# Kernel tuning notes

Hardware: AMD Instinct MI355X
Metric: run time of the kernel (lower is better)

The kernel has to match this reference:

```python
import jax, jax.numpy as jnp
import numpy as np

NUM_HEADS = 12
HEAD_SIZE = 64  # hidden 768 / 12 heads


def setup_inputs() -> dict:
    key = jax.random.key(0)
    ks = jax.random.split(key, 5)
    B, M, P, H = 8, 4, 512, 768
    scale = 1.0 / np.sqrt(H)
    return {
        "hidden_states": jax.random.normal(ks[0], (B, M, P, H), dtype=jnp.float32),
        "Wq": jax.random.normal(ks[1], (H, H), dtype=jnp.float32) * scale,
        "bq": jnp.zeros((H,), dtype=jnp.float32),
        "Wk": jax.random.normal(ks[2], (H, H), dtype=jnp.float32) * scale,
        "bk": jnp.zeros((H,), dtype=jnp.float32),
        "Wv": jax.random.normal(ks[3], (H, H), dtype=jnp.float32) * scale,
        "bv": jnp.zeros((H,), dtype=jnp.float32),
        "Wo": jax.random.normal(ks[4], (H, H), dtype=jnp.float32) * scale,
        "bo": jnp.zeros((H,), dtype=jnp.float32),
    }


def reference(hidden_states, Wq, bq, Wk, bk, Wv, bv, Wo, bo):
    # hidden_states: [B, M, P, H] (batch, modalities, patches, hidden)
    B, M, P, H = hidden_states.shape
    nh, hs = NUM_HEADS, HEAD_SIZE

    def split_heads(x):  # [B,M,P,H] -> [B,M,nh,P,hs]
        return x.reshape(B, M, P, nh, hs).transpose(0, 1, 3, 2, 4)

    q = split_heads(hidden_states @ Wq + bq)
    k = split_heads(hidden_states @ Wk + bk)
    v = split_heads(hidden_states @ Wv + bv)

    # per-modality, per-head attention over patches
    scores = jnp.einsum('bmnqh,bmnkh->bmnqk', q, k) / np.sqrt(hs).astype(jnp.float32)
    probs = jax.nn.softmax(scores, axis=-1)  # [B,M,nh,P,P]
    ctx = jnp.einsum('bmnqk,bmnkh->bmnqh', probs, v)
    ctx = ctx.transpose(0, 1, 3, 2, 4).reshape(B, M, P, H)  # merge heads

    # output projection (dropout rate 0.0 -> identity)
    return ctx @ Wo + bo
```

## Files before the change

### kernel.cpp

```cpp
#include <hip/hip_runtime.h>
#include <cstdint>
#include <cstddef>

#define H_DIM 768
#define NHEADS 12
#define HSZ 64
#define PATCH 512
#define MTOT 16384
#define SZT ((long)MTOT * H_DIM)

using short8 = __attribute__((ext_vector_type(8))) short;
using f32x4  = __attribute__((ext_vector_type(4))) float;
using us4    = __attribute__((ext_vector_type(4))) unsigned short;

#define GLL16(gp, lp) __builtin_amdgcn_global_load_lds( \
    (const __attribute__((address_space(1))) void*)(gp), \
    (__attribute__((address_space(3))) void*)(lp), 16, 0, 0)

__device__ __forceinline__ void split_f32(float x, unsigned short& h, unsigned short& l) {
    unsigned u = __float_as_uint(x);
    h = (unsigned short)(u >> 16);
    float rem = __uint_as_float(u & 0xffff0000u);
    float r = x - rem;
    unsigned v = __float_as_uint(r);
    v += 0x7fff + ((v >> 16) & 1);
    l = (unsigned short)(v >> 16);
}

__device__ __forceinline__ unsigned short bf16rne(float x) {
    unsigned v = __float_as_uint(x);
    v += 0x7fff + ((v >> 16) & 1);
    return (unsigned short)(v >> 16);
}

__global__ __launch_bounds__(256) void prep_x(const float* __restrict__ X,
                                              unsigned short* __restrict__ Xb)
{
    const long i = ((long)blockIdx.x * 256 + threadIdx.x) * 8;
    float4 a = *(const float4*)&X[i];
    float4 b = *(const float4*)&X[i + 4];
    float xs[8] = {a.x, a.y, a.z, a.w, b.x, b.y, b.z, b.w};
    us4 h0, h1;
    #pragma unroll
    for (int j = 0; j < 4; ++j) { h0[j] = bf16rne(xs[j]); h1[j] = bf16rne(xs[j + 4]); }
    *(us4*)&Xb[i] = h0; *(us4*)&Xb[i + 4] = h1;
}

template<int LO>
__global__ __launch_bounds__(256) void prep_w(const float* __restrict__ W,
                                              unsigned short* __restrict__ Whi,
                                              unsigned short* __restrict__ Wlo)
{
    __shared__ float T[64][65];
    const int kt = blockIdx.x * 64, nt = blockIdx.y * 64;
    const int tid = threadIdx.x;
    const int r = tid >> 2, c16 = (tid & 3) * 16;
    #pragma unroll
    for (int j = 0; j < 4; ++j) {
        float4 v = *(const float4*)&W[(long)(kt + r) * H_DIM + nt + c16 + j * 4];
        T[r][c16 + j*4 + 0] = v.x; T[r][c16 + j*4 + 1] = v.y;
        T[r][c16 + j*4 + 2] = v.z; T[r][c16 + j*4 + 3] = v.w;
    }
    __syncthreads();
    unsigned short* ph = &Whi[(long)(nt + r) * H_DIM + kt + c16];
    #pragma unroll
    for (int j = 0; j < 16; ++j) {
        if (LO) {
            unsigned short hh, ll;
            split_f32(T[c16 + j][r], hh, ll);
            ph[j] = hh;
            Wlo[(long)(nt + r) * H_DIM + kt + c16 + j] = ll;
        } else {
            ph[j] = bf16rne(T[c16 + j][r]);
        }
    }
}

__global__ __launch_bounds__(256, 2) void qkv_gemm(
    const unsigned short* __restrict__ Xb,
    const unsigned short* __restrict__ WqH, const unsigned short* __restrict__ WkH,
    const unsigned short* __restrict__ WvH,
    const float* __restrict__ bq, const float* __restrict__ bk, const float* __restrict__ bv,
    float qscale,
    unsigned short* __restrict__ Qt, unsigned short* __restrict__ Kp,
    unsigned short* __restrict__ Vp)
{
    __shared__ unsigned short As[16384];
    __shared__ unsigned short Bs[16384];

    const int s   = blockIdx.x + 18 * blockIdx.y;
    const int lid = (s & 7) * 288 + (s >> 3);
    const int bx  = lid % 18;
    const int by  = lid / 18;

    const int mat = bx / 6;
    const int n0  = (bx % 6) * 128;
    const int m0  = by * 128;
    const unsigned short* Bh = (mat == 0) ? WqH : (mat == 1) ? WkH : WvH;
    const float* bias        = (mat == 0) ? bq  : (mat == 1) ? bk  : bv;
    const float scale        = (mat == 0) ? qscale : 1.0f;

    const int tid  = threadIdx.x;
    const int lane = tid & 63;
    const int wv   = tid >> 6;
    const int wr   = wv >> 1, wc = wv & 1;
    const int q    = lane >> 4, l15 = lane & 15;

    const int srow   = tid >> 3;
    const int schunk = (tid & 7) ^ (srow & 7);

    char* ldsA = (char*)(&As[0]) + (wv << 10);
    char* ldsB = (char*)(&Bs[0]) + (wv << 10);

    f32x4 acc[4][4];
    #pragma unroll
    for (int i = 0; i < 4; ++i)
        #pragma unroll
        for (int j = 0; j < 4; ++j) acc[i][j] = 0;

    const int swz = (l15 & 7);

    #pragma unroll
    for (int i = 0; i < 4; ++i) {
        GLL16(Xb + (long)(m0 + i * 32 + srow) * H_DIM + schunk * 8, ldsA + i * 4096);
        GLL16(Bh + (long)(n0 + i * 32 + srow) * H_DIM + schunk * 8, ldsB + i * 4096);
    }

    int kb = 0;
    for (int k0 = 0; k0 < H_DIM; k0 += 64, kb ^= 1) {
        if (k0 + 64 < H_DIM) {
            #pragma unroll
            for (int i = 0; i < 4; ++i) {
                GLL16(Xb + (long)(m0 + i * 32 + srow) * H_DIM + (k0 + 64) + schunk * 8,
                      ldsA + ((kb ^ 1) << 14) + i * 4096);
                GLL16(Bh + (long)(n0 + i * 32 + srow) * H_DIM + (k0 + 64) + schunk * 8,
                      ldsB + ((kb ^ 1) << 14) + i * 4096);
            }
            asm volatile("s_waitcnt vmcnt(8)" ::: "memory");
        } else {
            asm volatile("s_waitcnt vmcnt(0)" ::: "memory");
        }
        __builtin_amdgcn_s_barrier();
        __builtin_amdgcn_sched_barrier(0);

        const unsigned short* Ab = &As[kb << 13];
        const unsigned short* Bb = &Bs[kb << 13];
        #pragma unroll
        for (int ks = 0; ks < 2; ++ks) {
            const int pc = ((ks * 4 + q) ^ swz) * 8;
            short8 ah[4], bh[4];
            #pragma unroll
            for (int t = 0; t < 4; ++t) {
                const int mr = wr * 64 + t * 16 + l15;
                ah[t] = *(const short8*)&Ab[mr * 64 + pc];
                const int nr = wc * 64 + t * 16 + l15;
                bh[t] = *(const short8*)&Bb[nr * 64 + pc];
            }
            #pragma unroll
            for (int mt = 0; mt < 4; ++mt)
                #pragma unroll
                for (int nt = 0; nt < 4; ++nt)
                    acc[mt][nt] = __builtin_amdgcn_mfma_f32_16x16x32_bf16(ah[mt], bh[nt], acc[mt][nt], 0, 0, 0);
        }
        asm volatile("s_waitcnt lgkmcnt(0)" ::: "memory");
        __builtin_amdgcn_sched_barrier(0);
        __builtin_amdgcn_s_barrier();
    }

    #pragma unroll
    for (int nt = 0; nt < 4; ++nt) {
        const int col = n0 + wc * 64 + nt * 16 + l15;
        const float bcol = bias[col];
        const int h = col >> 6, d = col & 63;
        #pragma unroll
        for (int mt = 0; mt < 4; ++mt) {
            const int rowB = m0 + wr * 64 + mt * 16 + q * 4;
            #pragma unroll
            for (int r = 0; r < 4; ++r) {
                const int row = rowB + r;
                const float val = (acc[mt][nt][r] + bcol) * scale;
                const int bm = row >> 9, p = row & 511;
                const int bmh = bm * NHEADS + h;
                if (mat == 0) {
                    const long idx = ((long)bmh * 8 + (p >> 6)) * 4096 + (long)(p & 63) * 64 + d;
                    Qt[idx] = bf16rne(val);
                } else if (mat == 1) {
                    Kp[(long)bmh * 32768 + (long)p * 64 + d] = bf16rne(val);
                } else {
                    Vp[(long)bmh * 32768 + (long)d * 512 + p] = bf16rne(val);
                }
            }
        }
    }
}

__global__ __launch_bounds__(256, 4) void attn2(
    const unsigned short* __restrict__ Qt,
    const unsigned short* __restrict__ Kp, const unsigned short* __restrict__ Vp,
    unsigned short* __restrict__ Ctx)
{
    __shared__ unsigned short Ks[4096];
    __shared__ unsigned short Vs[4096];
    __shared__ unsigned short Ps[128 * 72];
    __shared__ float red[128][2];

    const int tid  = threadIdx.x;
    const int lane = tid & 63;
    const int wv   = tid >> 6;
    const int wr   = wv >> 1, wc = wv & 1;
    const int q    = lane >> 4, l15 = lane & 15;

    const int s   = blockIdx.x + 4 * blockIdx.y;
    const int lid = (s & 7) * 192 + (s >> 3);
    const int qt2 = lid & 3;
    const int bmh = lid >> 2;

    short8 qh[4][2];
    const long qtile = ((long)bmh * 8 + qt2 * 2 + wr) * 4096;
    #pragma unroll
    for (int mt = 0; mt < 4; ++mt)
        #pragma unroll
        for (int ks = 0; ks < 2; ++ks)
            qh[mt][ks] = *(const short8*)&Qt[qtile + (mt * 16 + l15) * 64 + ks * 32 + q * 8];

    f32x4 ctx[4][2];
    float l_cur[4][4];
    #pragma unroll
    for (int mt = 0; mt < 4; ++mt) {
        ctx[mt][0] = 0; ctx[mt][1] = 0;
        #pragma unroll
        for (int r = 0; r < 4; ++r) l_cur[mt][r] = 0.0f;
    }

    const long khead = (long)bmh * 32768;
    const int srow   = tid >> 3;
    const int gchunk = ((tid & 7) ^ (srow & 7)) * 8;
    char* dK = (char*)&Ks[0] + (wv << 10);
    char* dV = (char*)&Vs[0] + (wv << 10);

    for (int kt = 0; kt < 8; ++kt) {
        __syncthreads();
        {
            const long kb = khead + (long)kt * 64 * 64;
            GLL16(Kp + kb + (long)srow * 64 + gchunk,        dK);
            GLL16(Kp + kb + (long)(srow + 32) * 64 + gchunk, dK + 4096);
            const long vb = khead + (long)kt * 64;
            GLL16(Vp + vb + (long)srow * 512 + gchunk,        dV);
            GLL16(Vp + vb + (long)(srow + 32) * 512 + gchunk, dV + 4096);
        }
        __syncthreads();

        f32x4 s[4][2];
        #pragma unroll
        for (int mt = 0; mt < 4; ++mt) { s[mt][0] = 0; s[mt][1] = 0; }
        short8 kf[2][2];
        #pragma unroll
        for (int nt = 0; nt < 2; ++nt)
            #pragma unroll
            for (int ks = 0; ks < 2; ++ks) {
                const int key = wc * 32 + nt * 16 + l15;
                const int phys = (q + ks * 4) ^ (key & 7);
                kf[nt][ks] = *(const short8*)&Ks[key * 64 + phys * 8];
            }
        #pragma unroll
        for (int mt = 0; mt < 4; ++mt)
            #pragma unroll
            for (int nt = 0; nt < 2; ++nt)
                #pragma unroll
                for (int ks = 0; ks < 2; ++ks)
                    s[mt][nt] = __builtin_amdgcn_mfma_f32_16x16x32_bf16(qh[mt][ks], kf[nt][ks], s[mt][nt], 0, 0, 0);

        #pragma unroll
        for (int mt = 0; mt < 4; ++mt)
            #pragma unroll
            for (int r = 0; r < 4; ++r) {
                const int row = wr * 64 + mt * 16 + q * 4 + r;
                const float p0 = __builtin_amdgcn_exp2f(s[mt][0][r]);
                const float p1 = __builtin_amdgcn_exp2f(s[mt][1][r]);
                l_cur[mt][r] += p0 + p1;
                Ps[row * 72 + wc * 32 + l15]      = bf16rne(p0);
                Ps[row * 72 + wc * 32 + 16 + l15] = bf16rne(p1);
            }
        __syncthreads();

        short8 pf[4][2], vf[2][2];
        #pragma unroll
        for (int mt = 0; mt < 4; ++mt)
            #pragma unroll
            for (int ks = 0; ks < 2; ++ks)
                pf[mt][ks] = *(const short8*)&Ps[(wr * 64 + mt * 16 + l15) * 72 + ks * 32 + q * 8];
        #pragma unroll
        for (int nt = 0; nt < 2; ++nt)
            #pragma unroll
            for (int ks = 0; ks < 2; ++ks) {
                const int d = wc * 32 + nt * 16 + l15;
                const int phys = (q + ks * 4) ^ (d & 7);
                vf[nt][ks] = *(const short8*)&Vs[d * 64 + phys * 8];
            }
        #pragma unroll
        for (int mt = 0; mt < 4; ++mt)
            #pragma unroll
            for (int nt = 0; nt < 2; ++nt)
                #pragma unroll
                for (int ks = 0; ks < 2; ++ks)
                    ctx[mt][nt] = __builtin_amdgcn_mfma_f32_16x16x32_bf16(pf[mt][ks], vf[nt][ks], ctx[mt][nt], 0, 0, 0);
    }

    #pragma unroll
    for (int mt = 0; mt < 4; ++mt)
        #pragma unroll
        for (int r = 0; r < 4; ++r) {
            float v = l_cur[mt][r];
            v += __shfl_xor(v, 1);
            v += __shfl_xor(v, 2);
            v += __shfl_xor(v, 4);
            v += __shfl_xor(v, 8);
            if (l15 == 0) red[wr * 64 + mt * 16 + q * 4 + r][wc] = v;
        }
    __syncthreads();
    #pragma unroll
    for (int mt = 0; mt < 4; ++mt)
        #pragma unroll
        for (int r = 0; r < 4; ++r) {
            const int row = wr * 64 + mt * 16 + q * 4 + r;
            const float2 rd = *(const float2*)&red[row][0];
            const float inv = 1.0f / (rd.x + rd.y);
            const int trow = mt * 16 + q * 4 + r;
            #pragma unroll
            for (int nt = 0; nt < 2; ++nt) {
                const int col = wc * 32 + nt * 16 + l15;
                Ctx[qtile + trow * 64 + col] = bf16rne(ctx[mt][nt][r] * inv);
            }
        }
}

__global__ __launch_bounds__(256, 3) void oproj(
    const unsigned short* __restrict__ Ctx,
    const unsigned short* __restrict__ WoH, const unsigned short* __restrict__ WoL,
    const float* __restrict__ bo, float* __restrict__ out)
{
    __shared__ unsigned short As[8192];
    __shared__ unsigned short Bs[2][8192];

    const int tid  = threadIdx.x;
    const int lane = tid & 63;
    const int wv   = tid >> 6;
    const int wr   = wv >> 1, wc = wv & 1;
    const int q    = lane >> 4, l15 = lane & 15;

    const int s   = blockIdx.x + 6 * blockIdx.y;
    const int lid = (s & 7) * 96 + (s >> 3);
    const int n0  = (lid % 6) * 128;
    const int m0  = (lid / 6) * 128;

    const int srow   = tid >> 3;
    const int schunk = (tid & 7) ^ (srow & 7);

    char* ldsA = (char*)(&As[0]) + (wv << 10);
    char* ldsB = (char*)(&Bs[0][0]) + (wv << 10);

    f32x4 acc[4][4];
    #pragma unroll
    for (int i = 0; i < 4; ++i)
        #pragma unroll
        for (int j = 0; j < 4; ++j) acc[i][j] = 0;

    const int swz = (l15 & 7);

    for (int k0 = 0; k0 < H_DIM; k0 += 64) {
        const int h = k0 >> 6;
        #pragma unroll
        for (int i = 0; i < 4; ++i) {
            const int tok = m0 + i * 32 + srow;
            const long tile = ((long)(tok >> 9) * NHEADS + h) * 8 + ((tok >> 6) & 7);
            GLL16(Ctx + tile * 4096 + (long)(tok & 63) * 64 + schunk * 8, ldsA + i * 4096);
            GLL16(WoH + (long)(n0 + i * 32 + srow) * H_DIM + k0 + schunk * 8, ldsB + i * 4096);
            GLL16(WoL + (long)(n0 + i * 32 + srow) * H_DIM + k0 + schunk * 8, ldsB + 16384 + i * 4096);
        }
        __syncthreads();

        #pragma unroll
        for (int ks = 0; ks < 2; ++ks) {
            const int pc = ((ks * 4 + q) ^ swz) * 8;
            short8 ah[4], bh[4], bl[4];
            #pragma unroll
            for (int t = 0; t < 4; ++t) {
                const int mr = wr * 64 + t * 16 + l15;
                ah[t] = *(const short8*)&As[mr * 64 + pc];
                const int nr = wc * 64 + t * 16 + l15;
                bh[t] = *(const short8*)&Bs[0][nr * 64 + pc];
                bl[t] = *(const short8*)&Bs[1][nr * 64 + pc];
            }
            #pragma unroll
            for (int mt = 0; mt < 4; ++mt)
                #pragma unroll
                for (int nt = 0; nt < 4; ++nt) {
                    acc[mt][nt] = __builtin_amdgcn_mfma_f32_16x16x32_bf16(ah[mt], bh[nt], acc[mt][nt], 0, 0, 0);
                    acc[mt][nt] = __builtin_amdgcn_mfma_f32_16x16x32_bf16(ah[mt], bl[nt], acc[mt][nt], 0, 0, 0);
                }
        }
        __syncthreads();
    }

    #pragma unroll
    for (int nt = 0; nt < 4; ++nt) {
        const int col = n0 + wc * 64 + nt * 16 + l15;
        const float bcol = bo[col];
        #pragma unroll
        for (int mt = 0; mt < 4; ++mt) {
            const int rowB = m0 + wr * 64 + mt * 16 + q * 4;
            #pragma unroll
            for (int r = 0; r < 4; ++r)
                out[(long)(rowB + r) * H_DIM + col] = acc[mt][nt][r] + bcol;
        }
    }
}

extern "C" void kernel_launch(void* const* d_in, const int* in_sizes, int n_in,
                              void* d_out, int out_size, void* d_ws, size_t ws_size,
                              hipStream_t stream) {
    const float* X  = (const float*)d_in[0];
    const float* Wq = (const float*)d_in[1]; const float* bq = (const float*)d_in[2];
    const float* Wk = (const float*)d_in[3]; const float* bk = (const float*)d_in[4];
    const float* Wv = (const float*)d_in[5]; const float* bv = (const float*)d_in[6];
    const float* Wo = (const float*)d_in[7]; const float* bo = (const float*)d_in[8];

    unsigned short* wsu = (unsigned short*)d_ws;
    unsigned short* Qt  = wsu;
    unsigned short* Kp  = Qt + 12582912L;
    unsigned short* Vp  = Kp + 12582912L;
    unsigned short* Wt  = Vp + 12582912L;
    const long WP = (long)H_DIM * H_DIM;
    unsigned short* WqH = Wt;
    unsigned short* WkH = Wt + WP;
    unsigned short* WvH = Wt + 2 * WP;
    unsigned short* WoH = Wt + 3 * WP;
    unsigned short* WoL = Wt + 4 * WP;

    unsigned short* Xb = (unsigned short*)d_out;

    prep_x<<<(int)(SZT / 2048), 256, 0, stream>>>(X, Xb);
    dim3 wgrid(12, 12);
    prep_w<0><<<wgrid, 256, 0, stream>>>(Wq, WqH, nullptr);
    prep_w<0><<<wgrid, 256, 0, stream>>>(Wk, WkH, nullptr);
    prep_w<0><<<wgrid, 256, 0, stream>>>(Wv, WvH, nullptr);
    prep_w<1><<<wgrid, 256, 0, stream>>>(Wo, WoH, WoL);

    const float qscale = 0.125f * 1.4426950408889634f;
    qkv_gemm<<<dim3(18, 128), 256, 0, stream>>>(Xb, WqH, WkH, WvH,
                                                bq, bk, bv, qscale, Qt, Kp, Vp);

    attn2<<<dim3(4, 384), 256, 0, stream>>>(Qt, Kp, Vp, Qt);

    oproj<<<dim3(6, 128), 256, 0, stream>>>(Qt, WoH, WoL, bo, (float*)d_out);
}
```

Measured before the change: 326.7 us.

## Restructure QKV GEMM into 256x128 tiles with triple-buffered interleaved prefetch

The QKV projection GEMM now runs 512-thread blocks on 256x128 output tiles, with 8 waves arranged 4x2. Shared memory is triple-buffered and global-to-LDS loads for tile k+2 are spread across the two half-K MFMA phases. Each phase adds barriers and raises wave priority around the MFMA block. The aim is to hide memory latency better and reuse each B tile across twice as many rows. In exchange the kernel uses more LDS per block (144 KB), so fewer blocks fit per CU, and the synchronisation is more intricate.

```diff
diff --git a/kernel.cpp b/kernel.cpp
--- a/kernel.cpp
+++ b/kernel.cpp
@@ -16,6 +16,8 @@
 #define GLL16(gp, lp) __builtin_amdgcn_global_load_lds( \
     (const __attribute__((address_space(1))) void*)(gp), \
     (__attribute__((address_space(3))) void*)(lp), 16, 0, 0)
+
+#define SB0() __builtin_amdgcn_sched_barrier(0)
 
 __device__ __forceinline__ void split_f32(float x, unsigned short& h, unsigned short& l) {
     unsigned u = __float_as_uint(x);
@@ -76,7 +78,7 @@
     }
 }
 
-__global__ __launch_bounds__(256, 2) void qkv_gemm(
+__global__ __launch_bounds__(512, 2) void qkv_gemm(
     const unsigned short* __restrict__ Xb,
     const unsigned short* __restrict__ WqH, const unsigned short* __restrict__ WkH,
     const unsigned short* __restrict__ WvH,
@@ -85,17 +87,18 @@
     unsigned short* __restrict__ Qt, unsigned short* __restrict__ Kp,
     unsigned short* __restrict__ Vp)
 {
-    __shared__ unsigned short As[16384];
-    __shared__ unsigned short Bs[16384];
-
-    const int s   = blockIdx.x + 18 * blockIdx.y;
-    const int lid = (s & 7) * 288 + (s >> 3);
-    const int bx  = lid % 18;
-    const int by  = lid / 18;
-
-    const int mat = bx / 6;
-    const int n0  = (bx % 6) * 128;
-    const int m0  = by * 128;
+    __shared__ unsigned short As[3 * 16384];
+    __shared__ unsigned short Bs[3 * 8192];
+
+    const int s    = blockIdx.x;
+    const int lid  = (s & 7) * 144 + (s >> 3);
+    const int mrow = lid / 18;
+    const int rest = lid % 18;
+    const int mat  = rest / 6;
+    const int ncol = rest % 6;
+    const int m0   = mrow * 256;
+    const int n0   = ncol * 128;
+
     const unsigned short* Bh = (mat == 0) ? WqH : (mat == 1) ? WkH : WvH;
     const float* bias        = (mat == 0) ? bq  : (mat == 1) ? bk  : bv;
     const float scale        = (mat == 0) ? qscale : 1.0f;
@@ -103,14 +106,20 @@
     const int tid  = threadIdx.x;
     const int lane = tid & 63;
     const int wv   = tid >> 6;
-    const int wr   = wv >> 1, wc = wv & 1;
+    const int wr   = wv >> 1;
+    const int wc   = wv & 1;
     const int q    = lane >> 4, l15 = lane & 15;
 
     const int srow   = tid >> 3;
     const int schunk = (tid & 7) ^ (srow & 7);
 
-    char* ldsA = (char*)(&As[0]) + (wv << 10);
-    char* ldsB = (char*)(&Bs[0]) + (wv << 10);
+    #define STAGE_A(buf, j, ko) GLL16(Xb + (long)(m0 + (j) * 64 + srow) * H_DIM + (ko) + schunk * 8, \
+                                      (char*)(buf) + (j) * 8192 + (wv << 10))
+    #define STAGE_B(buf, j, ko) GLL16(Bh + (long)(n0 + (j) * 64 + srow) * H_DIM + (ko) + schunk * 8, \
+                                      (char*)(buf) + (j) * 8192 + (wv << 10))
+
+    unsigned short *Ac = &As[0], *An = &As[16384], *At = &As[32768];
+    unsigned short *Bc = &Bs[0], *Bn = &Bs[8192],  *Bt = &Bs[16384];
 
     f32x4 acc[4][4];
     #pragma unroll
@@ -118,54 +127,77 @@
         #pragma unroll
         for (int j = 0; j < 4; ++j) acc[i][j] = 0;
 
-    const int swz = (l15 & 7);
-
-    #pragma unroll
-    for (int i = 0; i < 4; ++i) {
-        GLL16(Xb + (long)(m0 + i * 32 + srow) * H_DIM + schunk * 8, ldsA + i * 4096);
-        GLL16(Bh + (long)(n0 + i * 32 + srow) * H_DIM + schunk * 8, ldsB + i * 4096);
-    }
-
-    int kb = 0;
-    for (int k0 = 0; k0 < H_DIM; k0 += 64, kb ^= 1) {
-        if (k0 + 64 < H_DIM) {
-            #pragma unroll
-            for (int i = 0; i < 4; ++i) {
-                GLL16(Xb + (long)(m0 + i * 32 + srow) * H_DIM + (k0 + 64) + schunk * 8,
-                      ldsA + ((kb ^ 1) << 14) + i * 4096);
-                GLL16(Bh + (long)(n0 + i * 32 + srow) * H_DIM + (k0 + 64) + schunk * 8,
-                      ldsB + ((kb ^ 1) << 14) + i * 4096);
-            }
-            asm volatile("s_waitcnt vmcnt(8)" ::: "memory");
-        } else {
-            asm volatile("s_waitcnt vmcnt(0)" ::: "memory");
-        }
-        __builtin_amdgcn_s_barrier();
-        __builtin_amdgcn_sched_barrier(0);
-
-        const unsigned short* Ab = &As[kb << 13];
-        const unsigned short* Bb = &Bs[kb << 13];
-        #pragma unroll
-        for (int ks = 0; ks < 2; ++ks) {
-            const int pc = ((ks * 4 + q) ^ swz) * 8;
+    #pragma unroll
+    for (int j = 0; j < 4; ++j) STAGE_A(Ac, j, 0);
+    #pragma unroll
+    for (int j = 0; j < 2; ++j) STAGE_B(Bc, j, 0);
+    #pragma unroll
+    for (int j = 0; j < 4; ++j) STAGE_A(An, j, 64);
+    #pragma unroll
+    for (int j = 0; j < 2; ++j) STAGE_B(Bn, j, 64);
+    asm volatile("s_waitcnt vmcnt(6)" ::: "memory");
+    __builtin_amdgcn_s_barrier();
+
+    #pragma unroll 1
+    for (int kt = 0; kt < 12; ++kt) {
+        const long ko = (long)kt * 64 + 128;
+        const bool st = (kt < 10);
+
+        {
             short8 ah[4], bh[4];
             #pragma unroll
             for (int t = 0; t < 4; ++t) {
                 const int mr = wr * 64 + t * 16 + l15;
-                ah[t] = *(const short8*)&Ab[mr * 64 + pc];
+                ah[t] = *(const short8*)&Ac[mr * 64 + ((0 + q) ^ (l15 & 7)) * 8];
                 const int nr = wc * 64 + t * 16 + l15;
-                bh[t] = *(const short8*)&Bb[nr * 64 + pc];
-            }
+                bh[t] = *(const short8*)&Bc[nr * 64 + ((0 + q) ^ (l15 & 7)) * 8];
+            }
+            if (st) { STAGE_A(At, 0, ko); STAGE_A(At, 1, ko); STAGE_A(At, 2, ko); }
+            SB0();
+            __builtin_amdgcn_s_barrier();
+            asm volatile("s_waitcnt lgkmcnt(0)" ::: "memory");
+            SB0();
+            __builtin_amdgcn_s_setprio(1);
             #pragma unroll
             for (int mt = 0; mt < 4; ++mt)
                 #pragma unroll
                 for (int nt = 0; nt < 4; ++nt)
                     acc[mt][nt] = __builtin_amdgcn_mfma_f32_16x16x32_bf16(ah[mt], bh[nt], acc[mt][nt], 0, 0, 0);
-        }
-        asm volatile("s_waitcnt lgkmcnt(0)" ::: "memory");
-        __builtin_amdgcn_sched_barrier(0);
-        __builtin_amdgcn_s_barrier();
-    }
+            __builtin_amdgcn_s_setprio(0);
+            __builtin_amdgcn_s_barrier();
+        }
+
+        {
+            short8 ah[4], bh[4];
+            #pragma unroll
+            for (int t = 0; t < 4; ++t) {
+                const int mr = wr * 64 + t * 16 + l15;
+                ah[t] = *(const short8*)&Ac[mr * 64 + ((4 + q) ^ (l15 & 7)) * 8];
+                const int nr = wc * 64 + t * 16 + l15;
+                bh[t] = *(const short8*)&Bc[nr * 64 + ((4 + q) ^ (l15 & 7)) * 8];
+            }
+            if (st) { STAGE_A(At, 3, ko); STAGE_B(Bt, 0, ko); STAGE_B(Bt, 1, ko); }
+            SB0();
+            __builtin_amdgcn_s_barrier();
+            asm volatile("s_waitcnt lgkmcnt(0)" ::: "memory");
+            SB0();
+            __builtin_amdgcn_s_setprio(1);
+            #pragma unroll
+            for (int mt = 0; mt < 4; ++mt)
+                #pragma unroll
+                for (int nt = 0; nt < 4; ++nt)
+                    acc[mt][nt] = __builtin_amdgcn_mfma_f32_16x16x32_bf16(ah[mt], bh[nt], acc[mt][nt], 0, 0, 0);
+            __builtin_amdgcn_s_setprio(0);
+            if (st) asm volatile("s_waitcnt vmcnt(6)" ::: "memory");
+            else    asm volatile("s_waitcnt vmcnt(0)" ::: "memory");
+            __builtin_amdgcn_s_barrier();
+        }
+
+        unsigned short* ta = Ac; Ac = An; An = At; At = ta;
+        unsigned short* tb = Bc; Bc = Bn; Bn = Bt; Bt = tb;
+    }
+    #undef STAGE_A
+    #undef STAGE_B
 
     #pragma unroll
     for (int nt = 0; nt < 4; ++nt) {
@@ -447,8 +479,8 @@
     prep_w<1><<<wgrid, 256, 0, stream>>>(Wo, WoH, WoL);
 
     const float qscale = 0.125f * 1.4426950408889634f;
-    qkv_gemm<<<dim3(18, 128), 256, 0, stream>>>(Xb, WqH, WkH, WvH,
-                                                bq, bk, bv, qscale, Qt, Kp, Vp);
+    qkv_gemm<<<dim3(1152), 512, 0, stream>>>(Xb, WqH, WkH, WvH,
+                                             bq, bk, bv, qscale, Qt, Kp, Vp);
 
     attn2<<<dim3(4, 384), 256, 0, stream>>>(Qt, Kp, Vp, Qt);
 
```

Measured after the change: 335.4 us. 1.03x slower.
